# Kernel optimization log

Measured on AMD Instinct MI355X. Metric: run time of the kernel, lower is better.

Reference implementation:

```python
import jax, jax.numpy as jnp
import numpy as np

# Config: B=4, S=2048, E=512, H=8 heads, D=E//H=64, FF=2048.
# QLayer (quantum circuit) is replaced by its linear stand-in matching the
# declared I/O dims: V: D->D per head, Q/K: D->1 (scalar per token).

EPS = 1e-5

def layernorm(x):
    # torch LayerNorm(elementwise_affine=False), population variance
    mu = jnp.mean(x, axis=-1, keepdims=True)
    var = jnp.var(x, axis=-1, keepdims=True)
    return (x - mu) / jnp.sqrt(var + EPS)


def setup_inputs() -> dict:
    key = jax.random.key(0)
    ks = jax.random.split(key, 12)
    B, S, E, H = 4, 2048, 512, 8
    D = E // H
    F = 2048
    u = lambda k, shape, fan: jax.random.uniform(k, shape, jnp.float32, -1.0 / np.sqrt(fan), 1.0 / np.sqrt(fan))
    return {
        "input1": jax.random.normal(ks[0], (B, S, E), jnp.float32),
        # per-head value projection D->D
        "Wv": u(ks[1], (H, D, D), D),
        "bv": u(ks[2], (H, D), D),
        # per-head scalar query / key projections D->1
        "Wq": u(ks[3], (H, D), D),
        "bq": u(ks[4], (H,), D),
        "Wk": u(ks[5], (H, D), D),
        "bk": u(ks[6], (H,), D),
        # merger MLP: E->F (GELU) -> E
        "W1": u(ks[7], (E, F), E),
        "b1": u(ks[8], (F,), E),
        "W2": u(ks[9], (F, E), F),
        "b2": u(ks[10], (E,), F),
    }


def reference(input1, Wv, bv, Wq, bq, Wk, bk, W1, b1, W2, b2):
    B, S, E = input1.shape
    H, D, _ = Wv.shape
    x = layernorm(input1)
    # chunk along last dim == reshape into heads
    xh = x.reshape(B, S, H, D)
    # per-head projections (vectorized over heads)
    V = jnp.einsum('bshd,hde->bshe', xh, Wv) + bv            # [B,S,H,D]
    Q = jnp.einsum('bshd,hd->bhs', xh, Wq) + bq[None, :, None]  # [B,H,S]
    K = jnp.einsum('bshd,hd->bhs', xh, Wk) + bk[None, :, None]  # [B,H,S]
    # quadratic-distance scores: A = -(Q - K)^2, [B,H,S,S]
    A = -jnp.square(Q[:, :, :, None] - K[:, :, None, :])
    attn = jax.nn.softmax(A * (1.0 / np.sqrt(D)), axis=-1)
    head_out = jnp.einsum('bhqk,bkhd->bqhd', attn, V).reshape(B, S, E)
    # merger: Linear -> GELU (exact) -> Linear, plus residual
    h = jax.nn.gelu(head_out @ W1 + b1, approximate=False)
    return h @ W2 + b2 + input1
```

## Files before the change

### kernel.cpp

```cpp
#include <hip/hip_runtime.h>
#include <hip/hip_bf16.h>


#define Bsz 4
#define Ssz 2048
#define Esz 512
#define Hsz 8
#define Dsz 64
#define Fsz 2048
#define NR 16

typedef __attribute__((ext_vector_type(8))) short bf16x8;
typedef __attribute__((ext_vector_type(4))) float f32x4;

__device__ __constant__ float RS[16] = {
    0.f, 1.0f, 0.70710678f, 0.57735027f, 0.5f, 0.44721360f, 0.40824829f,
    0.37796447f, 0.35355339f, 0.33333333f, 0.31622777f, 0.30151134f,
    0.28867513f, 0.27735010f, 0.26726124f, 0.25819889f};

static __device__ __forceinline__ void gload_lds16(const void* g, void* l) {
    __builtin_amdgcn_global_load_lds(
        (const __attribute__((address_space(1))) unsigned int*)g,
        (__attribute__((address_space(3))) unsigned int*)l, 16, 0, 0);
}

static __device__ __forceinline__ unsigned short f2bf(float f) {
    unsigned int b = __float_as_uint(f);
    b += 0x7FFFu + ((b >> 16) & 1u);
    return (unsigned short)(b >> 16);
}
static __device__ __forceinline__ float bf2f(unsigned short u) {
    return __int_as_float(((int)u) << 16);
}

__global__ __launch_bounds__(256) void prep_kernel(
    const float* __restrict__ x,
    const float* __restrict__ Wq, const float* __restrict__ bq,
    const float* __restrict__ Wk, const float* __restrict__ bk,
    const float* __restrict__ W1, const float* __restrict__ W2,
    float* __restrict__ Qo, float* __restrict__ Ko, __hip_bfloat16* __restrict__ Xn,
    __hip_bfloat16* __restrict__ W1T, __hip_bfloat16* __restrict__ W2T)
{
    int bid = blockIdx.x;
    if (bid < 2048) {
        int wid = threadIdx.x >> 6, lane = threadIdx.x & 63;
        int tok = bid * 4 + wid;
        int b = tok >> 11, s = tok & 2047;

        const float* xrow = x + (size_t)tok * Esz;
        float4 v0 = *(const float4*)&xrow[lane * 8];
        float4 v1 = *(const float4*)&xrow[lane * 8 + 4];

        float sum = v0.x + v0.y + v0.z + v0.w + v1.x + v1.y + v1.z + v1.w;
        #pragma unroll
        for (int off = 32; off > 0; off >>= 1) sum += __shfl_xor(sum, off);
        float mean = sum * (1.0f / 512.0f);

        float d[8] = {v0.x - mean, v0.y - mean, v0.z - mean, v0.w - mean,
                      v1.x - mean, v1.y - mean, v1.z - mean, v1.w - mean};
        float ss = 0.f;
        #pragma unroll
        for (int j = 0; j < 8; ++j) ss = fmaf(d[j], d[j], ss);
        #pragma unroll
        for (int off = 32; off > 0; off >>= 1) ss += __shfl_xor(ss, off);
        float inv = rsqrtf(ss * (1.0f / 512.0f) + 1e-5f);

        float xn[8];
        #pragma unroll
        for (int j = 0; j < 8; ++j) xn[j] = d[j] * inv;

        int h = lane >> 3, dsub = (lane & 7) * 8;
        union { bf16x8 v; unsigned short u[8]; } pk;
        #pragma unroll
        for (int j = 0; j < 8; ++j) pk.u[j] = f2bf(xn[j]);
        *(bf16x8*)((unsigned short*)Xn + (((size_t)(b * Hsz + h) * Ssz + s) * Dsz + dsub)) = pk.v;

        float4 wqa = *(const float4*)&Wq[h * 64 + dsub];
        float4 wqb = *(const float4*)&Wq[h * 64 + dsub + 4];
        float4 wka = *(const float4*)&Wk[h * 64 + dsub];
        float4 wkb = *(const float4*)&Wk[h * 64 + dsub + 4];
        float pq = xn[0]*wqa.x + xn[1]*wqa.y + xn[2]*wqa.z + xn[3]*wqa.w
                 + xn[4]*wqb.x + xn[5]*wqb.y + xn[6]*wqb.z + xn[7]*wqb.w;
        float pkv = xn[0]*wka.x + xn[1]*wka.y + xn[2]*wka.z + xn[3]*wka.w
                  + xn[4]*wkb.x + xn[5]*wkb.y + xn[6]*wkb.z + xn[7]*wkb.w;
        #pragma unroll
        for (int off = 1; off < 8; off <<= 1) {
            pq  += __shfl_xor(pq, off);
            pkv += __shfl_xor(pkv, off);
        }
        if ((lane & 7) == 0) {
            int bh = b * Hsz + h;
            Qo[bh * Ssz + s] = pq + bq[h];
            Ko[bh * Ssz + s] = pkv + bk[h];
        }
        return;
    }

    __shared__ float tile[32][33];
    const float* in;
    __hip_bfloat16* outp;
    int R, C, bx, by;
    if (bid < 3072) {
        int tb = bid - 2048;
        in = W1; outp = W1T; R = Esz; C = Fsz;
        bx = tb & 63; by = tb >> 6;
    } else {
        int tb = bid - 3072;
        in = W2; outp = W2T; R = Fsz; C = Esz;
        bx = tb & 15; by = tb >> 4;
    }
    int t = threadIdx.x;
    int tc = t & 31, tr = t >> 5;
    #pragma unroll
    for (int i = 0; i < 4; ++i) {
        int rr = by * 32 + tr + i * 8, cc = bx * 32 + tc;
        tile[tr + i * 8][tc] = in[(size_t)rr * C + cc];
    }
    __syncthreads();
    #pragma unroll
    for (int i = 0; i < 4; ++i) {
        int ro = bx * 32 + tr + i * 8, co = by * 32 + tc;
        outp[(size_t)ro * R + co] = __float2bfloat16(tile[tc][tr + i * 8]);
    }
}

__global__ __launch_bounds__(512) void attn_moments_block(
    const float* __restrict__ Kv, const __hip_bfloat16* __restrict__ Xn,
    const float* __restrict__ Wv, const float* __restrict__ bvp,
    float* __restrict__ M)
{
    int bh = blockIdx.x, h = bh & 7;
    int t = threadIdx.x;
    __shared__ float Wt[512][17];
    __shared__ float Gf[NR * 68];

    int w = t >> 6, lane = t & 63;
    int kk = lane >> 3, dg = lane & 7;
    int ng = w * 2;
    float acc[2][8] = {};
    float dacc[2] = {};

    const unsigned short* xb = (const unsigned short*)Xn + (size_t)bh * Ssz * Dsz + dg * 8;

    for (int c = 0; c < Ssz / 512; ++c) {
        int k0 = c * 512;
        float kv = Kv[bh * Ssz + k0 + t];
        float wn = __expf(-0.125f * kv * kv);
        float half = 0.5f * kv;
        __syncthreads();
        Wt[t][0] = wn;
        #pragma unroll
        for (int n = 1; n < NR; ++n) { wn *= half * RS[n]; Wt[t][n] = wn; }
        __syncthreads();

        for (int kc = 0; kc < 512 / 8; ++kc) {
            int kl = kc * 8 + kk;
            bf16x8 xv = *(const bf16x8*)&xb[(size_t)(k0 + kl) * Dsz];
            float xf[8];
            #pragma unroll
            for (int e = 0; e < 8; ++e) xf[e] = bf2f((unsigned short)xv[e]);
            #pragma unroll
            for (int n = 0; n < 2; ++n) {
                float wt = Wt[kl][ng + n];
                dacc[n] += wt;
                #pragma unroll
                for (int e = 0; e < 8; ++e) acc[n][e] = fmaf(wt, xf[e], acc[n][e]);
            }
        }
    }

    #pragma unroll
    for (int off = 8; off < 64; off <<= 1) {
        #pragma unroll
        for (int n = 0; n < 2; ++n) {
            dacc[n] += __shfl_xor(dacc[n], off);
            #pragma unroll
            for (int e = 0; e < 8; ++e) acc[n][e] += __shfl_xor(acc[n][e], off);
        }
    }
    if (lane < 8) {
        #pragma unroll
        for (int n = 0; n < 2; ++n) {
            float* gp = &Gf[(ng + n) * 68 + dg * 8];
            float4 lo = {acc[n][0], acc[n][1], acc[n][2], acc[n][3]};
            float4 hi = {acc[n][4], acc[n][5], acc[n][6], acc[n][7]};
            *(float4*)gp = lo;
            *(float4*)(gp + 4) = hi;
        }
    }
    if (lane == 0) {
        #pragma unroll
        for (int n = 0; n < 2; ++n) Gf[(ng + n) * 68 + 64] = dacc[n];
    }
    __syncthreads();

    #pragma unroll
    for (int rep = 0; rep < 2; ++rep) {
        int o = t + rep * 512;
        int n = o >> 6, dd = o & 63;
        float den = Gf[n * 68 + 64];
        float accv = den * bvp[h * 64 + dd];
        const float* wv = Wv + ((size_t)h * 64) * 64 + dd;
        #pragma unroll
        for (int e = 0; e < 64; ++e) accv = fmaf(Gf[n * 68 + e], wv[(size_t)e * 64], accv);
        M[(size_t)bh * NR * 68 + n * 68 + dd] = accv;
        if (dd == 0) M[(size_t)bh * NR * 68 + n * 68 + 64] = den;
    }
}

__global__ __launch_bounds__(256) void attn_apply(
    const float* __restrict__ Qv, const float* __restrict__ M, __hip_bfloat16* __restrict__ A1)
{
    int tok = blockIdx.x;
    int b = tok >> 11, s = tok & 2047;
    int t = threadIdx.x;
    #pragma unroll
    for (int rep = 0; rep < 2; ++rep) {
        int e = t + rep * 256;
        int h = e >> 6, dd = e & 63;
        int bh = b * 8 + h;
        float q = Qv[bh * Ssz + s];
        const float* Mb = M + (size_t)bh * NR * 68;
        float half = 0.5f * q;
        float phi = 1.0f;
        float num = Mb[dd], den = Mb[64];
        #pragma unroll
        for (int n = 1; n < NR; ++n) {
            phi *= half * RS[n];
            num = fmaf(phi, Mb[n * 68 + dd], num);
            den = fmaf(phi, Mb[n * 68 + 64], den);
        }
        A1[(size_t)tok * Esz + e] = __float2bfloat16(num / den);
    }
}

template <int KDIM, int NDIM, int BN, int BK, int WRW, int EPI>
__global__ __launch_bounds__(512, 4) void gemm_bf16(
    const __hip_bfloat16* __restrict__ A, const __hip_bfloat16* __restrict__ Bt,
    const float* __restrict__ bias, const float* __restrict__ resid,
    void* __restrict__ Out)
{
    constexpr int NT = KDIM / BK;
    constexpr int WCW = 8 / WRW;
    constexpr int MROWS = 128 / WRW;
    constexpr int MF = MROWS / 16;
    constexpr int NCOLS = BN / WCW;
    constexpr int NF = NCOLS / 16;
    constexpr int KS = BK / 32;
    constexpr int NSLOT = BK / 8;
    constexpr int RPC = 4096 / BK;
    constexpr int ACALLS = 128 / RPC;
    constexpr int BCALLS = BN / RPC;
    constexpr int LPS = ACALLS + BCALLS;
    constexpr int NWGX = NDIM / BN;
    constexpr int NWG = NWGX * 64;

    __shared__ unsigned short As[3][128][BK];
    __shared__ unsigned short Bs[3][BN][BK];

    int t = threadIdx.x;
    int w = t >> 6, lane = t & 63;
    int wr = w / WCW, wc = w % WCW;

    int orig = blockIdx.x;
    int swzb = (orig & 7) * (NWG / 8) + (orig >> 3);
    int bm = (swzb / NWGX) * 128;
    int bn = (swzb % NWGX) * BN;

    f32x4 acc[MF][NF] = {};

    auto rswz = [](int r) -> int { return (BK == 32) ? ((r >> 1) & 3) : (r & 7); };

    const int tr = t / NSLOT;
    const int cgs = t & (NSLOT - 1);

    auto stage = [&](int kt, int buf) {
        int k0 = kt * BK;
        #pragma unroll
        for (int a = 0; a < ACALLS; ++a) {
            int r = a * RPC + tr;
            int srcc = cgs ^ rswz(r);
            gload_lds16(&A[(size_t)(bm + r) * KDIM + k0 + srcc * 8], &As[buf][r][cgs * 8]);
        }
        #pragma unroll
        for (int b = 0; b < BCALLS; ++b) {
            int r = b * RPC + tr;
            int srcc = cgs ^ rswz(r);
            gload_lds16(&Bt[(size_t)(bn + r) * KDIM + k0 + srcc * 8], &Bs[buf][r][cgs * 8]);
        }
    };
    auto wait_stage = [&](bool more_inflight) {
        if (more_inflight) {
            if constexpr (LPS == 2)      asm volatile("s_waitcnt vmcnt(2)" ::: "memory");
            else if constexpr (LPS == 3) asm volatile("s_waitcnt vmcnt(3)" ::: "memory");
            else                         asm volatile("s_waitcnt vmcnt(4)" ::: "memory");
        } else {
            asm volatile("s_waitcnt vmcnt(0)" ::: "memory");
        }
    };

    stage(0, 0);
    stage(1, 1);
    wait_stage(true);
    __builtin_amdgcn_s_barrier();
    __builtin_amdgcn_sched_barrier(0);

    const int l15 = lane & 15, lg = lane >> 4;

    for (int kt = 0; kt < NT; ++kt) {
        int cb = kt % 3;
        if (kt + 2 < NT) stage(kt + 2, (kt + 2) % 3);

        bf16x8 af[MF][KS], bfv[NF][KS];
        #pragma unroll
        for (int i = 0; i < MF; ++i) {
            int rr = wr * MROWS + i * 16 + l15;
            #pragma unroll
            for (int ks = 0; ks < KS; ++ks) {
                int slot = (lg + ks * 4) ^ rswz(rr);
                af[i][ks] = *(const bf16x8*)&As[cb][rr][slot * 8];
            }
        }
        #pragma unroll
        for (int j = 0; j < NF; ++j) {
            int rr = wc * NCOLS + j * 16 + l15;
            #pragma unroll
            for (int ks = 0; ks < KS; ++ks) {
                int slot = (lg + ks * 4) ^ rswz(rr);
                bfv[j][ks] = *(const bf16x8*)&Bs[cb][rr][slot * 8];
            }
        }
        __builtin_amdgcn_s_setprio(1);
        #pragma unroll
        for (int i = 0; i < MF; ++i)
            #pragma unroll
            for (int j = 0; j < NF; ++j)
                #pragma unroll
                for (int ks = 0; ks < KS; ++ks)
                    acc[i][j] = __builtin_amdgcn_mfma_f32_16x16x32_bf16(af[i][ks], bfv[j][ks], acc[i][j], 0, 0, 0);
        __builtin_amdgcn_s_setprio(0);

        if (kt + 1 < NT) {
            wait_stage(kt + 2 < NT);
            __builtin_amdgcn_s_barrier();
            __builtin_amdgcn_sched_barrier(0);
        }
    }

    int col0 = lane & 15, rowg = lane >> 4;
    #pragma unroll
    for (int i = 0; i < MF; ++i) {
        #pragma unroll
        for (int j = 0; j < NF; ++j) {
            #pragma unroll
            for (int v = 0; v < 4; ++v) {
                int m = bm + wr * MROWS + i * 16 + rowg * 4 + v;
                int n = bn + wc * NCOLS + j * 16 + col0;
                float val = acc[i][j][v] + bias[n];
                if (EPI == 0) {
                    float g = 0.5f * val * (1.0f + erff(val * 0.70710678f));
                    ((__hip_bfloat16*)Out)[(size_t)m * NDIM + n] = __float2bfloat16(g);
                } else {
                    size_t idx = (size_t)m * NDIM + n;
                    ((float*)Out)[idx] = val + resid[idx];
                }
            }
        }
    }
}

extern "C" void kernel_launch(void* const* d_in, const int* in_sizes, int n_in,
                              void* d_out, int out_size, void* d_ws, size_t ws_size,
                              hipStream_t stream) {
    const float* x  = (const float*)d_in[0];
    const float* Wv = (const float*)d_in[1];
    const float* bv = (const float*)d_in[2];
    const float* Wq = (const float*)d_in[3];
    const float* bq = (const float*)d_in[4];
    const float* Wk = (const float*)d_in[5];
    const float* bk = (const float*)d_in[6];
    const float* W1 = (const float*)d_in[7];
    const float* b1 = (const float*)d_in[8];
    const float* W2 = (const float*)d_in[9];
    const float* b2 = (const float*)d_in[10];
    float* out = (float*)d_out;

    char* ws = (char*)d_ws;
    float* Qb    = (float*)(ws + 0);
    float* Kb    = (float*)(ws + 262144);
    __hip_bfloat16* Xn = (__hip_bfloat16*)(ws + 524288);
    __hip_bfloat16* A1 = (__hip_bfloat16*)(ws + 8912896);
    float* Mfull = (float*)(ws + 17301504);
    __hip_bfloat16* W1T  = (__hip_bfloat16*)(ws + 17441024);
    __hip_bfloat16* W2T  = (__hip_bfloat16*)(ws + 19538176);
    __hip_bfloat16* hbuf = (__hip_bfloat16*)(ws + 21635328);

    prep_kernel<<<dim3(4096), 256, 0, stream>>>(x, Wq, bq, Wk, bk, W1, W2, Qb, Kb, Xn, W1T, W2T);
    attn_moments_block<<<dim3(Bsz * Hsz), 512, 0, stream>>>(Kb, Xn, Wv, bv, Mfull);
    attn_apply<<<dim3(Bsz * Ssz), 256, 0, stream>>>(Qb, Mfull, A1);
    gemm_bf16<Esz, Fsz, 256, 32, 2, 0><<<dim3(512), 512, 0, stream>>>(A1, W1T, b1, nullptr, hbuf);
    gemm_bf16<Fsz, Esz, 64, 64, 4, 1><<<dim3(512), 512, 0, stream>>>(hbuf, W2T, b2, x, out);
}
```

Measured before the change: 194.9 us.

## Replace first MLP GEMM with 256x256-tile, four-phase ping-pong scheduled kernel

Adds a dedicated GEMM kernel for the E->F projection with GELU. It uses 256x256 output tiles, BK=64 and double-buffered LDS filled by direct global-to-LDS loads. Each k-step is split into four MFMA quadrants, with prefetch loads interleaved between them, plus barriers and setprio to overlap memory with matrix math. Larger tiles raise data reuse, but the grid drops to 256 workgroups and LDS use grows to 128KB, so occupancy may fall.

Measured after the change: 201.6 us. 1.03x slower.

```diff
diff --git a/kernel.cpp b/kernel.cpp
--- a/kernel.cpp
+++ b/kernel.cpp
@@ -231,6 +231,133 @@
             den = fmaf(phi, Mb[n * 68 + 64], den);
         }
         A1[(size_t)tok * Esz + e] = __float2bfloat16(num / den);
+    }
+}
+
+
+#define QUAD_MFMA(MH, NH)                                                              \
+    _Pragma("unroll") for (int i = 0; i < 4; ++i)                                      \
+    _Pragma("unroll") for (int j = 0; j < 2; ++j)                                      \
+    _Pragma("unroll") for (int ks = 0; ks < 2; ++ks)                                   \
+        acc[(MH)*4 + i][(NH)*2 + j] = __builtin_amdgcn_mfma_f32_16x16x32_bf16(         \
+            af[i][ks], bfr[j][ks], acc[(MH)*4 + i][(NH)*2 + j], 0, 0, 0);
+
+#define READ_A(MH)                                                                     \
+    _Pragma("unroll") for (int i = 0; i < 4; ++i) {                                    \
+        int rr = wr * 128 + (MH)*64 + i * 16 + l15;                                    \
+        _Pragma("unroll") for (int ks = 0; ks < 2; ++ks) {                             \
+            int slot = (ks * 4 + lg) ^ (rr & 7);                                       \
+            af[i][ks] = *(const bf16x8*)&As1[db][rr][slot * 8];                        \
+        }                                                                              \
+    }
+
+#define READ_B(NH)                                                                     \
+    _Pragma("unroll") for (int j = 0; j < 2; ++j) {                                    \
+        int rr = wc * 64 + (NH)*32 + j * 16 + l15;                                     \
+        _Pragma("unroll") for (int ks = 0; ks < 2; ++ks) {                             \
+            int slot = (ks * 4 + lg) ^ (rr & 7);                                       \
+            bfr[j][ks] = *(const bf16x8*)&Bs1[db][rr][slot * 8];                       \
+        }                                                                              \
+    }
+
+#define PHASE_PRE                                                                      \
+    __builtin_amdgcn_sched_barrier(0);                                                 \
+    __builtin_amdgcn_s_barrier();                                                      \
+    asm volatile("s_waitcnt lgkmcnt(0)" ::: "memory");                                 \
+    __builtin_amdgcn_sched_barrier(0);                                                 \
+    __builtin_amdgcn_s_setprio(1);
+
+#define PHASE_POST                                                                     \
+    __builtin_amdgcn_s_setprio(0);                                                     \
+    __builtin_amdgcn_sched_barrier(0);                                                 \
+    __builtin_amdgcn_s_barrier();
+
+__global__ __launch_bounds__(512, 2) void gemm1_8ph(
+    const __hip_bfloat16* __restrict__ A, const __hip_bfloat16* __restrict__ Bt,
+    const float* __restrict__ bias, __hip_bfloat16* __restrict__ Out)
+{
+    constexpr int KDIM = 512, NDIM = 2048, NT1 = KDIM / 64;
+    constexpr int NWGX = NDIM / 256;
+    constexpr int NWG = NWGX * 32;
+
+    __shared__ unsigned short As1[2][256][64];
+    __shared__ unsigned short Bs1[2][256][64];
+
+    int t = threadIdx.x;
+    int w = t >> 6, lane = t & 63;
+    int wr = w >> 2, wc = w & 3;
+    const int l15 = lane & 15, lg = lane >> 4;
+
+    int orig = blockIdx.x;
+    int swzb = (orig & 7) * (NWG / 8) + (orig >> 3);
+    int bm = (swzb / NWGX) * 256;
+    int bn = (swzb % NWGX) * 256;
+
+    f32x4 acc[8][4] = {};
+
+    const int strow = t >> 3;
+    const int stslot = t & 7;
+
+    auto stage_q = [&](int kt, int buf, int q) {
+        int k0 = kt * 64;
+        int r = (q & 3) * 64 + strow;
+        int srcc = stslot ^ (r & 7);
+        if (q < 4)
+            gload_lds16(&A[(size_t)(bm + r) * KDIM + k0 + srcc * 8], &As1[buf][r][stslot * 8]);
+        else
+            gload_lds16(&Bt[(size_t)(bn + r) * KDIM + k0 + srcc * 8], &Bs1[buf][r][stslot * 8]);
+    };
+
+    #pragma unroll
+    for (int q = 0; q < 8; ++q) stage_q(0, 0, q);
+    asm volatile("s_waitcnt vmcnt(0)" ::: "memory");
+    __builtin_amdgcn_s_barrier();
+
+    for (int kt = 0; kt < NT1; ++kt) {
+        int db = kt & 1, nb = db ^ 1;
+        bool pf = (kt + 1 < NT1);
+        bf16x8 af[4][2], bfr[2][2];
+
+        READ_A(0) READ_B(0)
+        if (pf) { stage_q(kt + 1, nb, 0); stage_q(kt + 1, nb, 1); }
+        PHASE_PRE QUAD_MFMA(0, 0) PHASE_POST
+
+        READ_B(1)
+        if (pf) { stage_q(kt + 1, nb, 2); stage_q(kt + 1, nb, 3); }
+        PHASE_PRE QUAD_MFMA(0, 1) PHASE_POST
+
+        READ_A(1)
+        if (pf) { stage_q(kt + 1, nb, 4); stage_q(kt + 1, nb, 5); }
+        PHASE_PRE QUAD_MFMA(1, 1) PHASE_POST
+
+        READ_B(0)
+        if (pf) { stage_q(kt + 1, nb, 6); stage_q(kt + 1, nb, 7); }
+        __builtin_amdgcn_sched_barrier(0);
+        __builtin_amdgcn_s_barrier();
+        asm volatile("s_waitcnt lgkmcnt(0)" ::: "memory");
+        __builtin_amdgcn_sched_barrier(0);
+        __builtin_amdgcn_s_setprio(1);
+        QUAD_MFMA(1, 0)
+        __builtin_amdgcn_s_setprio(0);
+        __builtin_amdgcn_sched_barrier(0);
+        if (pf) asm volatile("s_waitcnt vmcnt(0)" ::: "memory");
+        __builtin_amdgcn_s_barrier();
+    }
+
+    int col0 = lane & 15, rowg = lane >> 4;
+    #pragma unroll
+    for (int ai = 0; ai < 8; ++ai) {
+        #pragma unroll
+        for (int bj = 0; bj < 4; ++bj) {
+            #pragma unroll
+            for (int v = 0; v < 4; ++v) {
+                int m = bm + wr * 128 + (ai >> 2) * 64 + (ai & 3) * 16 + rowg * 4 + v;
+                int n = bn + wc * 64 + (bj >> 1) * 32 + (bj & 1) * 16 + col0;
+                float val = acc[ai][bj][v] + bias[n];
+                float g = 0.5f * val * (1.0f + erff(val * 0.70710678f));
+                Out[(size_t)m * NDIM + n] = __float2bfloat16(g);
+            }
+        }
     }
 }
 
@@ -398,6 +525,6 @@
     prep_kernel<<<dim3(4096), 256, 0, stream>>>(x, Wq, bq, Wk, bk, W1, W2, Qb, Kb, Xn, W1T, W2T);
     attn_moments_block<<<dim3(Bsz * Hsz), 512, 0, stream>>>(Kb, Xn, Wv, bv, Mfull);
     attn_apply<<<dim3(Bsz * Ssz), 256, 0, stream>>>(Qb, Mfull, A1);
-    gemm_bf16<Esz, Fsz, 256, 32, 2, 0><<<dim3(512), 512, 0, stream>>>(A1, W1T, b1, nullptr, hbuf);
+    gemm1_8ph<<<dim3(256), 512, 0, stream>>>(A1, W1T, b1, hbuf);
     gemm_bf16<Fsz, Esz, 64, 64, 4, 1><<<dim3(512), 512, 0, stream>>>(hbuf, W2T, b2, x, out);
 }
```
